# Kernel tuning notes

Hardware: AMD Instinct MI355X
Metric: run time of the kernel (lower is better)

## Reference

```python
import jax, jax.numpy as jnp
import numpy as np

EMBED_DIM = 1024
HEADS = 16
HEAD_DIM = EMBED_DIM // HEADS


def setup_inputs() -> dict:
    key = jax.random.key(0)
    ks = jax.random.split(key, 5)
    B, N, C = 2, 2048, EMBED_DIM
    scale = 1.0 / np.sqrt(C)
    x = jax.random.normal(ks[0], (B, N, C), dtype=jnp.float32)
    W_qkv = jax.random.normal(ks[1], (C, 3 * C), dtype=jnp.float32) * scale
    b_qkv = jax.random.normal(ks[2], (3 * C,), dtype=jnp.float32) * 0.01
    W_out = jax.random.normal(ks[3], (C, C), dtype=jnp.float32) * scale
    b_out = jax.random.normal(ks[4], (C,), dtype=jnp.float32) * 0.01
    return {"x": x, "W_qkv": W_qkv, "b_qkv": b_qkv, "W_out": W_out, "b_out": b_out}


def reference(x, W_qkv, b_qkv, W_out, b_out):
    B, N, C = x.shape
    qkv = x @ W_qkv + b_qkv                      # [B, N, 3C]
    qkv = qkv.reshape(B, N, 3, HEADS, HEAD_DIM)
    qkv = jnp.transpose(qkv, (2, 0, 3, 1, 4))    # [3, B, H, N, d]
    q, k, v = qkv[0], qkv[1], qkv[2]
    attn = jnp.einsum('bhnd,bhmd->bhnm', q, k) / np.sqrt(HEAD_DIM)
    attn = jax.nn.softmax(attn, axis=-1)
    out = jnp.einsum('bhnm,bhmd->bhnd', attn, v)  # [B, H, N, d]
    out = jnp.transpose(out, (0, 2, 1, 3)).reshape(B, N, C)
    return out @ W_out + b_out
```

## Files before the change

kernel.cpp:

```cpp
#include <hip/hip_runtime.h>
#include <stdint.h>

typedef __bf16 bf16_t;
typedef bf16_t bf16x8 __attribute__((ext_vector_type(8)));
typedef bf16_t bf16x2v __attribute__((ext_vector_type(2)));
typedef short short4v __attribute__((ext_vector_type(4)));
typedef float f32x4 __attribute__((ext_vector_type(4)));
typedef uint32_t u32x2 __attribute__((ext_vector_type(2)));

#define BATCH 2
#define SEQ 2048
#define CDIM 1024
#define NH 16
#define HD 64

#define QSCALE 0.18033688011f

__device__ __forceinline__ uint16_t f32_bf16(float f) {
    __bf16 h = (__bf16)f;
    return __builtin_bit_cast(uint16_t, h);
}

__device__ __forceinline__ uint32_t pack_bf16(float a, float b) {
    bf16x2v t;
    t.x = (__bf16)a;
    t.y = (__bf16)b;
    return __builtin_bit_cast(uint32_t, t);
}

__device__ __forceinline__ bf16x8 ld8(const uint16_t* p) {
    return *reinterpret_cast<const bf16x8*>(p);
}

__device__ __forceinline__ void gld16(const uint16_t* g, uint16_t* l) {
    __builtin_amdgcn_global_load_lds(
        (__attribute__((address_space(1))) void*)(g),
        (__attribute__((address_space(3))) void*)(l), 16, 0, 0);
}

#define LDS_FENCE() asm volatile("s_waitcnt lgkmcnt(0)" ::: "memory")

__global__ __launch_bounds__(256) void prep_kernel(
        const float* __restrict__ x, uint16_t* __restrict__ x_bf,
        const float* __restrict__ Wqkv, uint16_t* __restrict__ wqkvT,
        const float* __restrict__ Wout, uint16_t* __restrict__ woutT) {
    const int bid = blockIdx.x, tid = threadIdx.x;
    if (bid < 4096) {
        int i = (bid * 256 + tid) * 4;
        float4 v = *(const float4*)(x + i);
        ushort4 o;
        o.x = f32_bf16(v.x);
        o.y = f32_bf16(v.y);
        o.z = f32_bf16(v.z);
        o.w = f32_bf16(v.w);
        *(ushort4*)(x_bf + i) = o;
        return;
    }
    __shared__ float tile[32][33];
    const float* in;
    uint16_t* outp;
    int idx, Cc, ncx;
    if (bid < 4096 + 3072) { idx = bid - 4096; in = Wqkv; outp = wqkvT; Cc = 3072; ncx = 96; }
    else                   { idx = bid - 7168; in = Wout; outp = woutT; Cc = 1024; ncx = 32; }
    const int R = 1024;
    int bx = idx % ncx, by = idx / ncx;
    int c0 = bx * 32, r0 = by * 32;
    int tx = tid & 31, ty = tid >> 5;
#pragma unroll
    for (int i = 0; i < 4; i++)
        tile[ty + i * 8][tx] = in[(size_t)(r0 + ty + i * 8) * Cc + c0 + tx];
    __syncthreads();
#pragma unroll
    for (int i = 0; i < 4; i++) {
        int rr = ty + i * 8;
        outp[(size_t)(c0 + rr) * R + r0 + tx] = f32_bf16(tile[tx][rr]);
    }
}

template <int BM, int BN, int MODE>
__global__ __launch_bounds__(256) void gemm_t(
        const uint16_t* __restrict__ A, const uint16_t* __restrict__ Bt, int K,
        const float* __restrict__ bias,
        uint16_t* __restrict__ qw, uint16_t* __restrict__ kw, uint16_t* __restrict__ vt,
        float* __restrict__ out) {
    constexpr int WT_M = BM / 2, WT_N = BN / 2;
    constexpr int MI = WT_M / 16, NJ = WT_N / 16;
    constexpr int ASEG_W = BM / 64, BSEG_W = BN / 64;
    constexpr int AB = 2 * BM * 32 + 2 * BN * 32;
    constexpr int TS = (MODE == 0) ? 4 * 64 * 68 : 0;
    constexpr int SM = AB > TS ? AB : TS;
    __shared__ uint16_t smem[SM];
    uint16_t* As = smem;
    uint16_t* Bs = smem + 2 * BM * 32;

    const int m0 = blockIdx.y * BM, n0 = blockIdx.x * BN;
    const int tid = threadIdx.x;
    const int w = tid >> 6, lane = tid & 63;
    const int quad = lane >> 4, l16 = lane & 15;
    const int wm = (w >> 1) * WT_M, wn = (w & 1) * WT_N;

    const int srow = lane >> 2;
    const int schunk = (lane & 3) ^ (srow & 3);

    const uint16_t* aP[ASEG_W];
    const uint16_t* bP[BSEG_W];
    int aL[ASEG_W], bL[BSEG_W];
#pragma unroll
    for (int s = 0; s < ASEG_W; s++) {
        int seg = w * ASEG_W + s;
        aP[s] = A + (size_t)(m0 + seg * 16 + srow) * K + schunk * 8;
        aL[s] = seg * 512;
    }
#pragma unroll
    for (int s = 0; s < BSEG_W; s++) {
        int seg = w * BSEG_W + s;
        bP[s] = Bt + (size_t)(n0 + seg * 16 + srow) * K + schunk * 8;
        bL[s] = seg * 512;
    }

    auto stage = [&](int buf, int k0) {
#pragma unroll
        for (int s = 0; s < ASEG_W; s++) gld16(aP[s] + k0, As + buf * BM * 32 + aL[s]);
#pragma unroll
        for (int s = 0; s < BSEG_W; s++) gld16(bP[s] + k0, Bs + buf * BN * 32 + bL[s]);
    };

    const int cslot = (quad ^ (l16 & 3)) * 8;
    f32x4 acc[MI][NJ] = {};

    stage(0, 0);
    const int iters = K / 32;
    for (int it = 0; it < iters; ++it) {
        __syncthreads();
        if (it + 1 < iters) stage((it + 1) & 1, (it + 1) * 32);
        const uint16_t* A_ = As + (it & 1) * BM * 32;
        const uint16_t* B_ = Bs + (it & 1) * BN * 32;
        bf16x8 af[MI], bfr[NJ];
#pragma unroll
        for (int i = 0; i < MI; i++) af[i] = ld8(&A_[(wm + i * 16 + l16) * 32 + cslot]);
#pragma unroll
        for (int j = 0; j < NJ; j++) bfr[j] = ld8(&B_[(wn + j * 16 + l16) * 32 + cslot]);
#pragma unroll
        for (int i = 0; i < MI; i++)
#pragma unroll
            for (int j = 0; j < NJ; j++)
                acc[i][j] = __builtin_amdgcn_mfma_f32_16x16x32_bf16(af[i], bfr[j], acc[i][j], 0, 0, 0);
    }

    const int nbase = n0 + wn;
    float bj[NJ];
#pragma unroll
    for (int j = 0; j < NJ; j++) bj[j] = bias[nbase + j * 16 + l16];

    if constexpr (MODE == 1) {
#pragma unroll
        for (int j = 0; j < NJ; j++) {
#pragma unroll
            for (int i = 0; i < MI; i++)
#pragma unroll
                for (int r = 0; r < 4; r++) {
                    int m = m0 + wm + i * 16 + quad * 4 + r;
                    out[(size_t)m * CDIM + nbase + j * 16 + l16] = acc[i][j][r] + bj[j];
                }
        }
    } else {
        __syncthreads();
        uint16_t* T = smem + w * 64 * 68;
        const int gmb = m0 + wm;
        const int b = gmb >> 11, ns0 = gmb & 2047;

        if (nbase < 2048) {
            const int which = nbase >> 10, h = (nbase & 1023) >> 6;
            const float sc = (which == 0) ? QSCALE : 1.0f;
#pragma unroll
            for (int i = 0; i < 4; i++)
#pragma unroll
                for (int j = 0; j < 4; j++)
#pragma unroll
                    for (int r = 0; r < 4; r++)
                        T[(i * 16 + quad * 4 + r) * 68 + j * 16 + l16] =
                            f32_bf16((acc[i][j][r] + bj[j]) * sc);
            LDS_FENCE();
            uint16_t* dst = ((which == 0) ? qw : kw) +
                            (((size_t)b * NH + h) * SEQ + ns0 + lane) * HD;
#pragma unroll
            for (int g = 0; g < 8; g++) {
                bf16x8 v = ld8(&T[lane * 68 + g * 8]);
                *(bf16x8*)(dst + g * 8) = v;
            }
        } else {
#pragma unroll
            for (int i = 0; i < 4; i++)
#pragma unroll
                for (int j = 0; j < 4; j++) {
                    u32x2 pr;
                    pr.x = pack_bf16(acc[i][j][0] + bj[j], acc[i][j][1] + bj[j]);
                    pr.y = pack_bf16(acc[i][j][2] + bj[j], acc[i][j][3] + bj[j]);
                    *(u32x2*)&T[(j * 16 + l16) * 68 + i * 16 + quad * 4] = pr;
                }
            LDS_FENCE();
            const int h = (nbase - 2048) >> 6;
            uint16_t* dst = vt + (((size_t)b * NH + h) * HD + lane) * SEQ + ns0;
#pragma unroll
            for (int g = 0; g < 16; g++) {
                u32x2 d2 = *(const u32x2*)&T[lane * 68 + g * 4];
                int npos = (g & 3) * 16 + (g >> 2) * 4;
                *(u32x2*)(dst + npos) = d2;
            }
        }
    }
}

__global__ __launch_bounds__(256) void attn_kernel(
        const uint16_t* __restrict__ qg, const uint16_t* __restrict__ kg,
        const uint16_t* __restrict__ vt, uint16_t* __restrict__ og) {
    __shared__ uint16_t Ks[2][64 * 64];
    __shared__ uint16_t Vs[2][64 * 64];

    const int bh = blockIdx.x;
    const int qt = blockIdx.y;
    const int tid = threadIdx.x;
    const int w = tid >> 6, lane = tid & 63;
    const int quad = lane >> 4, l16 = lane & 15;
    const int qrow0 = qt * 64 + w * 16;
    const size_t base = (size_t)bh * SEQ * HD;

    bf16x8 qf[2];
#pragma unroll
    for (int ks = 0; ks < 2; ks++)
        qf[ks] = ld8(qg + base + (size_t)(qrow0 + l16) * HD + ks * 32 + quad * 8);

    const int srow = lane >> 3;
    const int schunk = (lane & 7) ^ srow;
    const int seg0 = w * 2, seg1 = seg0 + 1;
    const uint16_t* ksrc0 = kg + base + (size_t)(seg0 * 8 + srow) * HD + schunk * 8;
    const uint16_t* ksrc1 = kg + base + (size_t)(seg1 * 8 + srow) * HD + schunk * 8;
    const uint16_t* vsrc0 = vt + base + (size_t)(seg0 * 8 + srow) * SEQ + schunk * 8;
    const uint16_t* vsrc1 = vt + base + (size_t)(seg1 * 8 + srow) * SEQ + schunk * 8;
    const int soff0 = seg0 * 512, soff1 = seg1 * 512;

    f32x4 o_acc[4] = {};
    f32x4 l_acc = {};
    const short4v ones = { (short)0x3F80, (short)0x3F80, (short)0x3F80, (short)0x3F80 };

    gld16(ksrc0, &Ks[0][soff0]); gld16(ksrc1, &Ks[0][soff1]);
    gld16(vsrc0, &Vs[0][soff0]); gld16(vsrc1, &Vs[0][soff1]);
    ksrc0 += 64 * HD; ksrc1 += 64 * HD; vsrc0 += 64; vsrc1 += 64;

    for (int it = 0; it < SEQ / 64; ++it) {
        __syncthreads();
        if (it + 1 < SEQ / 64) {
            int pb = (it + 1) & 1;
            gld16(ksrc0, &Ks[pb][soff0]); gld16(ksrc1, &Ks[pb][soff1]);
            gld16(vsrc0, &Vs[pb][soff0]); gld16(vsrc1, &Vs[pb][soff1]);
            ksrc0 += 64 * HD; ksrc1 += 64 * HD; vsrc0 += 64; vsrc1 += 64;
        }
        const uint16_t* K_ = Ks[it & 1];
        const uint16_t* V_ = Vs[it & 1];

        f32x4 S[4] = {};
#pragma unroll
        for (int nf = 0; nf < 4; nf++) {
#pragma unroll
            for (int ks = 0; ks < 2; ks++) {
                bf16x8 kf = ld8(&K_[(nf * 16 + l16) * 64 + (((ks * 4 + quad) ^ (l16 & 7)) * 8)]);
                S[nf] = __builtin_amdgcn_mfma_f32_16x16x32_bf16(kf, qf[ks], S[nf], 0, 0, 0);
            }
        }

        uint32_t pk[4][2];
#pragma unroll
        for (int nf = 0; nf < 4; nf++) {
            float p0 = __builtin_amdgcn_exp2f(S[nf][0]);
            float p1 = __builtin_amdgcn_exp2f(S[nf][1]);
            float p2 = __builtin_amdgcn_exp2f(S[nf][2]);
            float p3 = __builtin_amdgcn_exp2f(S[nf][3]);
            pk[nf][0] = pack_bf16(p0, p1);
            pk[nf][1] = pack_bf16(p2, p3);
        }

#pragma unroll
        for (int kc = 0; kc < 4; kc++) {
            short4v pfrag = __builtin_bit_cast(short4v, (u32x2){pk[kc][0], pk[kc][1]});
            l_acc = __builtin_amdgcn_mfma_f32_16x16x16bf16_1k(ones, pfrag, l_acc, 0, 0, 0);
        }

#pragma unroll
        for (int mf = 0; mf < 4; mf++) {
            const int ro = (mf * 16 + l16) * 64;
            uint4 v0 = *(const uint4*)&V_[ro + (((quad * 2 + 0) ^ (l16 & 7)) * 8)];
            uint4 v1 = *(const uint4*)&V_[ro + (((quad * 2 + 1) ^ (l16 & 7)) * 8)];
            short4v vf[4];
            vf[0] = __builtin_bit_cast(short4v, (u32x2){v0.x, v0.y});
            vf[1] = __builtin_bit_cast(short4v, (u32x2){v0.z, v0.w});
            vf[2] = __builtin_bit_cast(short4v, (u32x2){v1.x, v1.y});
            vf[3] = __builtin_bit_cast(short4v, (u32x2){v1.z, v1.w});
#pragma unroll
            for (int kc = 0; kc < 4; kc++) {
                short4v pfrag = __builtin_bit_cast(short4v, (u32x2){pk[kc][0], pk[kc][1]});
                o_acc[mf] = __builtin_amdgcn_mfma_f32_16x16x16bf16_1k(vf[kc], pfrag, o_acc[mf], 0, 0, 0);
            }
        }
    }

    const int b = bh >> 4, h = bh & 15;
    const float inv = __builtin_amdgcn_rcpf(l_acc[0]);
    const int ns = qrow0 + l16;
    uint16_t* orow = og + (((size_t)b * SEQ + ns) * NH + h) * HD + quad * 4;
#pragma unroll
    for (int mf = 0; mf < 4; mf++) {
        ushort4 o;
        o.x = f32_bf16(o_acc[mf][0] * inv);
        o.y = f32_bf16(o_acc[mf][1] * inv);
        o.z = f32_bf16(o_acc[mf][2] * inv);
        o.w = f32_bf16(o_acc[mf][3] * inv);
        *(ushort4*)(orow + mf * 16) = o;
    }
}

extern "C" void kernel_launch(void* const* d_in, const int* in_sizes, int n_in,
                              void* d_out, int out_size, void* d_ws, size_t ws_size,
                              hipStream_t stream) {
    const float* x = (const float*)d_in[0];
    const float* Wqkv = (const float*)d_in[1];
    const float* bqkv = (const float*)d_in[2];
    const float* Wout = (const float*)d_in[3];
    const float* bout = (const float*)d_in[4];
    float* out = (float*)d_out;

    uint16_t* ws = (uint16_t*)d_ws;
    uint16_t* x_bf  = ws;
    uint16_t* wqkvT = x_bf + 4194304;
    uint16_t* woutT = wqkvT + 3145728;
    uint16_t* qw    = woutT + 1048576;
    uint16_t* kw    = qw + 4194304;
    uint16_t* vtw   = kw + 4194304;
    uint16_t* attn  = vtw + 4194304;

    prep_kernel<<<8192, 256, 0, stream>>>(x, x_bf, Wqkv, wqkvT, Wout, woutT);

    gemm_t<128, 128, 0><<<dim3(24, 32), 256, 0, stream>>>(
        x_bf, wqkvT, 1024, bqkv, qw, kw, vtw, nullptr);

    attn_kernel<<<dim3(32, 32), 256, 0, stream>>>(qw, kw, vtw, attn);

    gemm_t<64, 128, 1><<<dim3(8, 64), 256, 0, stream>>>(
        attn, woutT, 1024, bout, nullptr, nullptr, nullptr, out);
}
```

Measured before the change: 192.1 us.

## Process two query row groups per wave in attention to reuse K/V fragments

Each wave now handles 32 query rows instead of 16, so each attention block covers 128 query rows and the grid's query dimension is halved. K and V fragments loaded from shared memory are reused across two MFMA groups, which halves LDS traffic and the global K/V loads per query row. The cost is more accumulator registers per thread and only 512 blocks in the grid, which may lower occupancy and leave parts of the GPU idle.

```diff
diff --git a/kernel.cpp b/kernel.cpp
--- a/kernel.cpp
+++ b/kernel.cpp
@@ -222,13 +222,15 @@
     const int tid = threadIdx.x;
     const int w = tid >> 6, lane = tid & 63;
     const int quad = lane >> 4, l16 = lane & 15;
-    const int qrow0 = qt * 64 + w * 16;
+    const int qrow0 = qt * 128 + w * 32;
     const size_t base = (size_t)bh * SEQ * HD;
 
-    bf16x8 qf[2];
-#pragma unroll
-    for (int ks = 0; ks < 2; ks++)
-        qf[ks] = ld8(qg + base + (size_t)(qrow0 + l16) * HD + ks * 32 + quad * 8);
+    bf16x8 qf[2][2];
+#pragma unroll
+    for (int mg = 0; mg < 2; mg++)
+#pragma unroll
+        for (int ks = 0; ks < 2; ks++)
+            qf[mg][ks] = ld8(qg + base + (size_t)(qrow0 + mg * 16 + l16) * HD + ks * 32 + quad * 8);
 
     const int srow = lane >> 3;
     const int schunk = (lane & 7) ^ srow;
@@ -239,8 +241,8 @@
     const uint16_t* vsrc1 = vt + base + (size_t)(seg1 * 8 + srow) * SEQ + schunk * 8;
     const int soff0 = seg0 * 512, soff1 = seg1 * 512;
 
-    f32x4 o_acc[4] = {};
-    f32x4 l_acc = {};
+    f32x4 o_acc[2][4] = {};
+    f32x4 l_acc[2] = {};
     const short4v ones = { (short)0x3F80, (short)0x3F80, (short)0x3F80, (short)0x3F80 };
 
     gld16(ksrc0, &Ks[0][soff0]); gld16(ksrc1, &Ks[0][soff1]);
@@ -258,32 +260,38 @@
         const uint16_t* K_ = Ks[it & 1];
         const uint16_t* V_ = Vs[it & 1];
 
-        f32x4 S[4] = {};
+        f32x4 S[2][4] = {};
 #pragma unroll
         for (int nf = 0; nf < 4; nf++) {
 #pragma unroll
             for (int ks = 0; ks < 2; ks++) {
                 bf16x8 kf = ld8(&K_[(nf * 16 + l16) * 64 + (((ks * 4 + quad) ^ (l16 & 7)) * 8)]);
-                S[nf] = __builtin_amdgcn_mfma_f32_16x16x32_bf16(kf, qf[ks], S[nf], 0, 0, 0);
-            }
-        }
-
-        uint32_t pk[4][2];
-#pragma unroll
-        for (int nf = 0; nf < 4; nf++) {
-            float p0 = __builtin_amdgcn_exp2f(S[nf][0]);
-            float p1 = __builtin_amdgcn_exp2f(S[nf][1]);
-            float p2 = __builtin_amdgcn_exp2f(S[nf][2]);
-            float p3 = __builtin_amdgcn_exp2f(S[nf][3]);
-            pk[nf][0] = pack_bf16(p0, p1);
-            pk[nf][1] = pack_bf16(p2, p3);
-        }
-
-#pragma unroll
-        for (int kc = 0; kc < 4; kc++) {
-            short4v pfrag = __builtin_bit_cast(short4v, (u32x2){pk[kc][0], pk[kc][1]});
-            l_acc = __builtin_amdgcn_mfma_f32_16x16x16bf16_1k(ones, pfrag, l_acc, 0, 0, 0);
-        }
+#pragma unroll
+                for (int mg = 0; mg < 2; mg++)
+                    S[mg][nf] = __builtin_amdgcn_mfma_f32_16x16x32_bf16(kf, qf[mg][ks], S[mg][nf], 0, 0, 0);
+            }
+        }
+
+        uint32_t pk[2][4][2];
+#pragma unroll
+        for (int mg = 0; mg < 2; mg++)
+#pragma unroll
+            for (int nf = 0; nf < 4; nf++) {
+                float p0 = __builtin_amdgcn_exp2f(S[mg][nf][0]);
+                float p1 = __builtin_amdgcn_exp2f(S[mg][nf][1]);
+                float p2 = __builtin_amdgcn_exp2f(S[mg][nf][2]);
+                float p3 = __builtin_amdgcn_exp2f(S[mg][nf][3]);
+                pk[mg][nf][0] = pack_bf16(p0, p1);
+                pk[mg][nf][1] = pack_bf16(p2, p3);
+            }
+
+#pragma unroll
+        for (int mg = 0; mg < 2; mg++)
+#pragma unroll
+            for (int kc = 0; kc < 4; kc++) {
+                short4v pfrag = __builtin_bit_cast(short4v, (u32x2){pk[mg][kc][0], pk[mg][kc][1]});
+                l_acc[mg] = __builtin_amdgcn_mfma_f32_16x16x16bf16_1k(ones, pfrag, l_acc[mg], 0, 0, 0);
+            }
 
 #pragma unroll
         for (int mf = 0; mf < 4; mf++) {
@@ -296,25 +304,30 @@
             vf[2] = __builtin_bit_cast(short4v, (u32x2){v1.x, v1.y});
             vf[3] = __builtin_bit_cast(short4v, (u32x2){v1.z, v1.w});
 #pragma unroll
-            for (int kc = 0; kc < 4; kc++) {
-                short4v pfrag = __builtin_bit_cast(short4v, (u32x2){pk[kc][0], pk[kc][1]});
-                o_acc[mf] = __builtin_amdgcn_mfma_f32_16x16x16bf16_1k(vf[kc], pfrag, o_acc[mf], 0, 0, 0);
-            }
+            for (int kc = 0; kc < 4; kc++)
+#pragma unroll
+                for (int mg = 0; mg < 2; mg++) {
+                    short4v pfrag = __builtin_bit_cast(short4v, (u32x2){pk[mg][kc][0], pk[mg][kc][1]});
+                    o_acc[mg][mf] = __builtin_amdgcn_mfma_f32_16x16x16bf16_1k(vf[kc], pfrag, o_acc[mg][mf], 0, 0, 0);
+                }
         }
     }
 
     const int b = bh >> 4, h = bh & 15;
-    const float inv = __builtin_amdgcn_rcpf(l_acc[0]);
-    const int ns = qrow0 + l16;
-    uint16_t* orow = og + (((size_t)b * SEQ + ns) * NH + h) * HD + quad * 4;
-#pragma unroll
-    for (int mf = 0; mf < 4; mf++) {
-        ushort4 o;
-        o.x = f32_bf16(o_acc[mf][0] * inv);
-        o.y = f32_bf16(o_acc[mf][1] * inv);
-        o.z = f32_bf16(o_acc[mf][2] * inv);
-        o.w = f32_bf16(o_acc[mf][3] * inv);
-        *(ushort4*)(orow + mf * 16) = o;
+#pragma unroll
+    for (int mg = 0; mg < 2; mg++) {
+        const float inv = __builtin_amdgcn_rcpf(l_acc[mg][0]);
+        const int ns = qrow0 + mg * 16 + l16;
+        uint16_t* orow = og + (((size_t)b * SEQ + ns) * NH + h) * HD + quad * 4;
+#pragma unroll
+        for (int mf = 0; mf < 4; mf++) {
+            ushort4 o;
+            o.x = f32_bf16(o_acc[mg][mf][0] * inv);
+            o.y = f32_bf16(o_acc[mg][mf][1] * inv);
+            o.z = f32_bf16(o_acc[mg][mf][2] * inv);
+            o.w = f32_bf16(o_acc[mg][mf][3] * inv);
+            *(ushort4*)(orow + mf * 16) = o;
+        }
     }
 }
 
@@ -342,7 +355,7 @@
     gemm_t<128, 128, 0><<<dim3(24, 32), 256, 0, stream>>>(
         x_bf, wqkvT, 1024, bqkv, qw, kw, vtw, nullptr);
 
-    attn_kernel<<<dim3(32, 32), 256, 0, stream>>>(qw, kw, vtw, attn);
+    attn_kernel<<<dim3(32, 16), 256, 0, stream>>>(qw, kw, vtw, attn);
 
     gemm_t<64, 128, 1><<<dim3(8, 64), 256, 0, stream>>>(
         attn, woutT, 1024, bout, nullptr, nullptr, nullptr, out);
```

Measured after the change: 189.8 us. About the same (-1.2%).
